# Kernel optimization log

Measured on AMD Instinct MI355X. Metric: run time of the kernel, lower is better.

Reference implementation:

```python
import jax, jax.numpy as jnp
import numpy as np

N_NODES = 100000
N_EDGES = 3200000
F_IN, H_ENC, H_GCN, H_Q, A_DIM = 128, 128, 128, 256, 10


def setup_inputs() -> dict:
    key = jax.random.key(0)
    ks = jax.random.split(key, 8)
    s = lambda d: 1.0 / np.sqrt(d)
    return {
        "x": jax.random.normal(ks[0], (N_NODES, F_IN), jnp.float32),
        "edge_index": jax.random.randint(ks[1], (2, N_EDGES), 0, N_NODES, jnp.int64),
        "W_enc": jax.random.normal(ks[2], (F_IN, H_ENC), jnp.float32) * s(F_IN),
        "b_enc": jnp.zeros((H_ENC,), jnp.float32),
        "W_gcn": jax.random.normal(ks[3], (H_ENC, H_GCN), jnp.float32) * s(H_ENC),
        "b_gcn": jnp.zeros((H_GCN,), jnp.float32),
        "W1": jax.random.normal(ks[4], (H_GCN, H_Q), jnp.float32) * s(H_GCN),
        "b1": jnp.zeros((H_Q,), jnp.float32),
        "W2": jax.random.normal(ks[5], (H_Q, A_DIM), jnp.float32) * s(H_Q),
        "b2": jnp.zeros((A_DIM,), jnp.float32),
    }


def gcn_conv(x, edge_index, W, b):
    # Standard GCNConv: D^{-1/2} (A + I) D^{-1/2} X W + b, symmetric norm with self-loops.
    n = x.shape[0]
    src, dst = edge_index[0], edge_index[1]
    xw = x @ W  # [N, H]
    deg = jnp.ones((n,), xw.dtype).at[dst].add(1.0)  # in-degree + self-loop
    dinv = jax.lax.rsqrt(deg)
    coef = dinv[src] * dinv[dst]  # [E]
    msg = xw[src] * coef[:, None]  # [E, H] gather-scale
    agg = jax.ops.segment_sum(msg, dst, num_segments=n)  # scatter-add
    agg = agg + xw * (dinv * dinv)[:, None]  # self-loop contribution
    return agg + b


def reference(x, edge_index, W_enc, b_enc, W_gcn, b_gcn, W1, b1, W2, b2):
    h = jax.nn.relu(x @ W_enc + b_enc)              # Encoder: Linear + ReLU
    h = jax.nn.relu(gcn_conv(h, edge_index, W_gcn, b_gcn))  # GCNConv + ReLU
    q = jax.nn.relu(h @ W1 + b1) @ W2 + b2          # Q_Net MLP
    return q
```

## Files before the change

### kernel.cpp

```cpp
#include <hip/hip_runtime.h>

#define N_NODES 100000
constexpr int F     = 128;
constexpr int NB    = (N_NODES + 63) / 64;
constexpr int BCAP  = 2560;
constexpr int LCAP  = 80;
constexpr int CHUNK = 8192;
constexpr int PADN  = N_NODES;

typedef __attribute__((ext_vector_type(8))) short short8;
typedef __attribute__((ext_vector_type(4))) float f32x4;
typedef __attribute__((ext_vector_type(4))) short short4v;
typedef __attribute__((ext_vector_type(4))) unsigned uint4v;

__device__ inline short f2bf(float v) {
    union { float f; unsigned u; } x; x.f = v;
    unsigned r = (x.u + 0x7fff + ((x.u >> 16) & 1)) >> 16;
    return (short)r;
}
__device__ inline float lo_bf(unsigned v) {
    union { unsigned u; float f; } x; x.u = v << 16; return x.f;
}
__device__ inline float hi_bf(unsigned v) {
    union { unsigned u; float f; } x; x.u = v & 0xffff0000u; return x.f;
}

__global__ __launch_bounds__(256) void prep_kernel(const float* __restrict__ W_enc,
                                                   const float* __restrict__ W_gcn,
                                                   const float* __restrict__ W1,
                                                   const float* __restrict__ W2,
                                                   short* __restrict__ Wte,
                                                   short* __restrict__ Wtg,
                                                   short* __restrict__ Wt1,
                                                   short* __restrict__ W2t,
                                                   int* __restrict__ bcr) {
    int idx = blockIdx.x * 256 + threadIdx.x;
    if (idx < 16384) { int h = idx >> 7, k = idx & 127; Wte[idx] = f2bf(W_enc[k * 128 + h]); return; }
    idx -= 16384;
    if (idx < 16384) { int h = idx >> 7, k = idx & 127; Wtg[idx] = f2bf(W_gcn[k * 128 + h]); return; }
    idx -= 16384;
    if (idx < 32768) { int h = idx >> 7, k = idx & 127; Wt1[idx] = f2bf(W1[k * 256 + h]); return; }
    idx -= 32768;
    if (idx < 4096)  { int n = idx >> 8, k = idx & 255; W2t[idx] = (n < 10) ? f2bf(W2[k * 10 + n]) : (short)0; return; }
    idx -= 4096;
    if (idx < NB) bcr[idx] = 0;
}

__global__ __launch_bounds__(512) void part_kernel(const int* __restrict__ src,
                                                   const int* __restrict__ dst,
                                                   int* __restrict__ bcur,
                                                   int* __restrict__ part, int E) {
    __shared__ int cnt[NB];
    __shared__ int base[NB];
    for (int b = threadIdx.x; b < NB; b += 512) cnt[b] = 0;
    __syncthreads();
    const int e0 = blockIdx.x * CHUNK;
    const int e1 = min(e0 + CHUNK, E);
#pragma unroll 4
    for (int e = e0 + threadIdx.x; e < e1; e += 512)
        atomicAdd(&cnt[dst[e] >> 6], 1);
    __syncthreads();
    for (int b = threadIdx.x; b < NB; b += 512) {
        int c = cnt[b];
        base[b] = c ? atomicAdd(&bcur[b], c) : 0;
        cnt[b] = 0;
    }
    __syncthreads();
#pragma unroll 4
    for (int e = e0 + threadIdx.x; e < e1; e += 512) {
        int d = dst[e];
        int b = d >> 6;
        int idx = base[b] + atomicAdd(&cnt[b], 1);
        if (idx < BCAP) part[b * BCAP + idx] = src[e] | ((d & 63) << 17);
    }
}

__global__ __launch_bounds__(256) void gemmA_kernel(const float* __restrict__ x,
                                                    const short* __restrict__ Wte,
                                                    const short* __restrict__ Wtg,
                                                    const float* __restrict__ b_enc,
                                                    const int* __restrict__ bcur,
                                                    const int* __restrict__ part,
                                                    short* __restrict__ xs) {
    __shared__ int deg_l[64];
    __shared__ short h_l[4][16][136];
    const int b = blockIdx.x;
    if (threadIdx.x < 64) deg_l[threadIdx.x] = 0;
    __syncthreads();
    const int cnt = min(bcur[b], BCAP);
    const int* p = part + (size_t)b * BCAP;
#pragma unroll 4
    for (int i = threadIdx.x; i < cnt; i += 256)
        atomicAdd(&deg_l[(p[i] >> 17) & 63], 1);

    const int wave = threadIdx.x >> 6;
    const int lane = threadIdx.x & 63;
    const int quad = lane >> 4;
    const int l16  = lane & 15;
    const int node0 = b * 64 + wave * 16;
    int nrow = node0 + l16;
    const bool valid = nrow < N_NODES;
    if (!valid) nrow = N_NODES - 1;

    f32x4 acc[8] = {};
#pragma unroll
    for (int kc = 0; kc < 4; ++kc) {
        const float* ap = x + (size_t)nrow * 128 + kc * 32 + quad * 8;
        float4 f0 = *reinterpret_cast<const float4*>(ap);
        float4 f1 = *reinterpret_cast<const float4*>(ap + 4);
        short8 xfrag;
        xfrag.s0 = f2bf(f0.x); xfrag.s1 = f2bf(f0.y); xfrag.s2 = f2bf(f0.z); xfrag.s3 = f2bf(f0.w);
        xfrag.s4 = f2bf(f1.x); xfrag.s5 = f2bf(f1.y); xfrag.s6 = f2bf(f1.z); xfrag.s7 = f2bf(f1.w);
#pragma unroll
        for (int t = 0; t < 8; ++t) {
            short8 wfrag = *reinterpret_cast<const short8*>(Wte + (size_t)(t * 16 + l16) * 128 + kc * 32 + quad * 8);
            acc[t] = __builtin_amdgcn_mfma_f32_16x16x32_bf16(wfrag, xfrag, acc[t], 0, 0, 0);
        }
    }
#pragma unroll
    for (int t = 0; t < 8; ++t) {
        short4v o;
#pragma unroll
        for (int r = 0; r < 4; ++r)
            ((short*)&o)[r] = f2bf(fmaxf(acc[t][r] + b_enc[t * 16 + quad * 4 + r], 0.f));
        *reinterpret_cast<short4v*>(&h_l[wave][l16][t * 16 + quad * 4]) = o;
    }
    __syncthreads();

    const float dvn = rsqrtf(1.f + (float)deg_l[wave * 16 + l16]);
    f32x4 acc2[8] = {};
#pragma unroll
    for (int kc = 0; kc < 4; ++kc) {
        short8 xfrag = *reinterpret_cast<const short8*>(&h_l[wave][l16][kc * 32 + quad * 8]);
#pragma unroll
        for (int t = 0; t < 8; ++t) {
            short8 wfrag = *reinterpret_cast<const short8*>(Wtg + (size_t)(t * 16 + l16) * 128 + kc * 32 + quad * 8);
            acc2[t] = __builtin_amdgcn_mfma_f32_16x16x32_bf16(wfrag, xfrag, acc2[t], 0, 0, 0);
        }
    }
    const int srow = node0 + l16;
#pragma unroll
    for (int t = 0; t < 8; ++t) {
        short4v o;
#pragma unroll
        for (int r = 0; r < 4; ++r)
            ((short*)&o)[r] = valid ? f2bf(acc2[t][r] * dvn) : (short)0;
        *reinterpret_cast<short4v*>(xs + (size_t)srow * 128 + t * 16 + quad * 4) = o;
    }
}

__global__ __launch_bounds__(512, 8) void agg_kernel(const short* __restrict__ xs,
                                                     const int* __restrict__ bcur,
                                                     const int* __restrict__ part,
                                                     const float* __restrict__ bg,
                                                     short* __restrict__ h2) {
    __shared__ int csr_l[64 * LCAP];
    __shared__ int cur[64];
    const int b = blockIdx.x;
    const int tid = threadIdx.x;
    if (tid < 64) cur[tid] = 0;
    __syncthreads();
    const int cnt = min(bcur[b], BCAP);
    const int* p = part + (size_t)b * BCAP;
#pragma unroll 4
    for (int i = tid; i < cnt; i += 512) {
        int v = p[i];
        int ld = (v >> 17) & 63;
        int pos = atomicAdd(&cur[ld], 1);
        if (pos < LCAP) csr_l[ld * LCAP + pos] = v & 0x1FFFF;
    }
    __syncthreads();
    if (tid < 64) {
        int d = min(cur[tid], LCAP);
        int dp = (d + 15) & ~15;
        for (int k = d; k < dp; ++k) csr_l[tid * LCAP + k] = PADN;
    }
    __syncthreads();

    const int wave = tid >> 6;
    const int lane = tid & 63;
    const int g    = lane >> 4;
    const int l16  = lane & 15;
    const uint4v* xs4 = reinterpret_cast<const uint4v*>(xs);
    const float4 bgA = reinterpret_cast<const float4*>(bg)[l16 * 2];
    const float4 bgB = reinterpret_cast<const float4*>(bg)[l16 * 2 + 1];

    for (int t = 0; t < 8; ++t) {
        const int ld = wave * 8 + t;
        const int node = b * 64 + ld;
        if (node >= N_NODES) break;

        const int dtrue = cur[ld];
        const int dpad = (min(dtrue, LCAP) + 15) & ~15;
        const float dv = rsqrtf(1.f + (float)dtrue);
        const int* cl = csr_l + ld * LCAP;

        float a0 = 0.f, a1 = 0.f, a2 = 0.f, a3 = 0.f, a4 = 0.f, a5 = 0.f, a6 = 0.f, a7 = 0.f;
        for (int j = 0; j < dpad; j += 16) {
            int s[4];
            uint4v v[4];
#pragma unroll
            for (int u = 0; u < 4; ++u) s[u] = cl[j + u * 4 + g];
#pragma unroll
            for (int u = 0; u < 4; ++u) v[u] = xs4[((size_t)s[u] << 4) + l16];
#pragma unroll
            for (int u = 0; u < 4; ++u) {
                a0 += lo_bf(v[u].x); a1 += hi_bf(v[u].x);
                a2 += lo_bf(v[u].y); a3 += hi_bf(v[u].y);
                a4 += lo_bf(v[u].z); a5 += hi_bf(v[u].z);
                a6 += lo_bf(v[u].w); a7 += hi_bf(v[u].w);
            }
        }
        a0 += __shfl_xor(a0, 16, 64); a0 += __shfl_xor(a0, 32, 64);
        a1 += __shfl_xor(a1, 16, 64); a1 += __shfl_xor(a1, 32, 64);
        a2 += __shfl_xor(a2, 16, 64); a2 += __shfl_xor(a2, 32, 64);
        a3 += __shfl_xor(a3, 16, 64); a3 += __shfl_xor(a3, 32, 64);
        a4 += __shfl_xor(a4, 16, 64); a4 += __shfl_xor(a4, 32, 64);
        a5 += __shfl_xor(a5, 16, 64); a5 += __shfl_xor(a5, 32, 64);
        a6 += __shfl_xor(a6, 16, 64); a6 += __shfl_xor(a6, 32, 64);
        a7 += __shfl_xor(a7, 16, 64); a7 += __shfl_xor(a7, 32, 64);
        if (g == 0) {
            uint4v vs = xs4[((size_t)node << 4) + l16];
            a0 += lo_bf(vs.x); a1 += hi_bf(vs.x);
            a2 += lo_bf(vs.y); a3 += hi_bf(vs.y);
            a4 += lo_bf(vs.z); a5 += hi_bf(vs.z);
            a6 += lo_bf(vs.w); a7 += hi_bf(vs.w);
            short8 o;
            o.s0 = f2bf(fmaxf(fmaf(a0, dv, bgA.x), 0.f));
            o.s1 = f2bf(fmaxf(fmaf(a1, dv, bgA.y), 0.f));
            o.s2 = f2bf(fmaxf(fmaf(a2, dv, bgA.z), 0.f));
            o.s3 = f2bf(fmaxf(fmaf(a3, dv, bgA.w), 0.f));
            o.s4 = f2bf(fmaxf(fmaf(a4, dv, bgB.x), 0.f));
            o.s5 = f2bf(fmaxf(fmaf(a5, dv, bgB.y), 0.f));
            o.s6 = f2bf(fmaxf(fmaf(a6, dv, bgB.z), 0.f));
            o.s7 = f2bf(fmaxf(fmaf(a7, dv, bgB.w), 0.f));
            *reinterpret_cast<short8*>(h2 + ((size_t)node << 7) + l16 * 8) = o;
        }
    }
}

__global__ __launch_bounds__(256) void gemmB_kernel(const short* __restrict__ h2,
                                                    const short* __restrict__ Wt1,
                                                    const short* __restrict__ W2t,
                                                    const float* __restrict__ b1,
                                                    const float* __restrict__ b2,
                                                    float* __restrict__ q) {
    __shared__ short hq_l[4][16][264];
    const int wave = threadIdx.x >> 6;
    const int lane = threadIdx.x & 63;
    const int quad = lane >> 4;
    const int l16  = lane & 15;
    const int node0 = blockIdx.x * 64 + wave * 16;
    int nrow = node0 + l16;
    if (nrow >= N_NODES) nrow = N_NODES - 1;

    f32x4 acc[16] = {};
#pragma unroll
    for (int kc = 0; kc < 4; ++kc) {
        short8 xfrag = *reinterpret_cast<const short8*>(h2 + (size_t)nrow * 128 + kc * 32 + quad * 8);
#pragma unroll
        for (int t = 0; t < 16; ++t) {
            short8 wfrag = *reinterpret_cast<const short8*>(Wt1 + (size_t)(t * 16 + l16) * 128 + kc * 32 + quad * 8);
            acc[t] = __builtin_amdgcn_mfma_f32_16x16x32_bf16(wfrag, xfrag, acc[t], 0, 0, 0);
        }
    }
#pragma unroll
    for (int t = 0; t < 16; ++t) {
        short4v o;
#pragma unroll
        for (int r = 0; r < 4; ++r)
            ((short*)&o)[r] = f2bf(fmaxf(acc[t][r] + b1[t * 16 + quad * 4 + r], 0.f));
        *reinterpret_cast<short4v*>(&hq_l[wave][l16][t * 16 + quad * 4]) = o;
    }

    f32x4 a2 = {};
#pragma unroll
    for (int kc = 0; kc < 8; ++kc) {
        short8 afrag = *reinterpret_cast<const short8*>(&hq_l[wave][l16][kc * 32 + quad * 8]);
        short8 bfrag = *reinterpret_cast<const short8*>(W2t + (size_t)l16 * 256 + kc * 32 + quad * 8);
        a2 = __builtin_amdgcn_mfma_f32_16x16x32_bf16(afrag, bfrag, a2, 0, 0, 0);
    }
    if (l16 < 10) {
        float bv = b2[l16];
#pragma unroll
        for (int r = 0; r < 4; ++r) {
            int nd = node0 + quad * 4 + r;
            if (nd < N_NODES) q[(size_t)nd * 10 + l16] = a2[r] + bv;
        }
    }
}

extern "C" void kernel_launch(void* const* d_in, const int* in_sizes, int n_in,
                              void* d_out, int out_size, void* d_ws, size_t ws_size,
                              hipStream_t stream) {
    const float* x     = (const float*)d_in[0];
    const int*   ei    = (const int*)d_in[1];
    const float* W_enc = (const float*)d_in[2];
    const float* b_enc = (const float*)d_in[3];
    const float* W_gcn = (const float*)d_in[4];
    const float* b_gcn = (const float*)d_in[5];
    const float* W1    = (const float*)d_in[6];
    const float* b1    = (const float*)d_in[7];
    const float* W2    = (const float*)d_in[8];
    const float* b2    = (const float*)d_in[9];
    float* q = (float*)d_out;

    const int E = in_sizes[1] / 2;
    const int* srcv = ei;
    const int* dstv = ei + E;

    char* ws = (char*)d_ws;
    const size_t XSB = (size_t)(NB * 64) * 128 * sizeof(short);
    short* xs  = (short*)(ws);
    short* h2  = (short*)(ws + XSB);
    int*   part= (int*)  (ws + 2 * XSB);
    char*  tail = ws + 2 * XSB + (size_t)NB * BCAP * sizeof(int);
    int*   bcr = (int*)(tail);
    short* Wte = (short*)(tail + 8192);
    short* Wtg = (short*)(tail + 8192 + 32768);
    short* Wt1 = (short*)(tail + 8192 + 65536);
    short* W2t = (short*)(tail + 8192 + 131072);

    prep_kernel<<<279, 256, 0, stream>>>(W_enc, W_gcn, W1, W2, Wte, Wtg, Wt1, W2t, bcr);
    part_kernel<<<(E + CHUNK - 1) / CHUNK, 512, 0, stream>>>(srcv, dstv, bcr, part, E);
    gemmA_kernel<<<NB, 256, 0, stream>>>(x, Wte, Wtg, b_enc, bcr, part, xs);
    agg_kernel<<<NB, 512, 0, stream>>>(xs, bcr, part, b_gcn, h2);
    gemmB_kernel<<<NB, 256, 0, stream>>>(h2, Wt1, W2t, b1, b2, q);
}
```

Baseline: 397.9 us.

## Cache edge data in registers during partition and double node rows in gemmB

The partition kernel now reads src/dst only once. It keeps the packed edge value and its local slot (bucket and position from the shared-memory atomic) in registers across the barrier. This removes the second global read pass and the second round of shared atomics, at the cost of 32 extra registers per thread. gemmB now processes 32 nodes per wave, so each W1 fragment load feeds two MFMAs, which halves weight-fragment traffic per node. In exchange it doubles accumulator register use and halves the number of blocks.

```diff
diff --git a/kernel.cpp b/kernel.cpp
--- a/kernel.cpp
+++ b/kernel.cpp
@@ -6,6 +6,7 @@
 constexpr int BCAP  = 2560;
 constexpr int LCAP  = 80;
 constexpr int CHUNK = 8192;
+constexpr int EPT   = CHUNK / 512;
 constexpr int PADN  = N_NODES;
 
 typedef __attribute__((ext_vector_type(8))) short short8;
@@ -46,32 +47,44 @@
     if (idx < NB) bcr[idx] = 0;
 }
 
-__global__ __launch_bounds__(512) void part_kernel(const int* __restrict__ src,
-                                                   const int* __restrict__ dst,
-                                                   int* __restrict__ bcur,
-                                                   int* __restrict__ part, int E) {
+__global__ __launch_bounds__(512, 4) void part_kernel(const int* __restrict__ src,
+                                                      const int* __restrict__ dst,
+                                                      int* __restrict__ bcur,
+                                                      int* __restrict__ part, int E) {
     __shared__ int cnt[NB];
     __shared__ int base[NB];
     for (int b = threadIdx.x; b < NB; b += 512) cnt[b] = 0;
     __syncthreads();
     const int e0 = blockIdx.x * CHUNK;
     const int e1 = min(e0 + CHUNK, E);
-#pragma unroll 4
-    for (int e = e0 + threadIdx.x; e < e1; e += 512)
-        atomicAdd(&cnt[dst[e] >> 6], 1);
+
+    int pk[EPT];
+    int meta[EPT];
+#pragma unroll
+    for (int i = 0; i < EPT; ++i) {
+        int e = e0 + i * 512 + (int)threadIdx.x;
+        meta[i] = -1;
+        if (e < e1) {
+            int d = dst[e];
+            int b = d >> 6;
+            pk[i] = src[e] | ((d & 63) << 17);
+            int pos = atomicAdd(&cnt[b], 1);
+            meta[i] = b | (pos << 11);
+        }
+    }
     __syncthreads();
     for (int b = threadIdx.x; b < NB; b += 512) {
         int c = cnt[b];
         base[b] = c ? atomicAdd(&bcur[b], c) : 0;
-        cnt[b] = 0;
-    }
-    __syncthreads();
-#pragma unroll 4
-    for (int e = e0 + threadIdx.x; e < e1; e += 512) {
-        int d = dst[e];
-        int b = d >> 6;
-        int idx = base[b] + atomicAdd(&cnt[b], 1);
-        if (idx < BCAP) part[b * BCAP + idx] = src[e] | ((d & 63) << 17);
+    }
+    __syncthreads();
+#pragma unroll
+    for (int i = 0; i < EPT; ++i) {
+        if (meta[i] >= 0) {
+            int b = meta[i] & 0x7FF;
+            int idx = base[b] + (meta[i] >> 11);
+            if (idx < BCAP) part[b * BCAP + idx] = pk[i];
+        }
     }
 }
 
@@ -250,42 +263,53 @@
     const int lane = threadIdx.x & 63;
     const int quad = lane >> 4;
     const int l16  = lane & 15;
-    const int node0 = blockIdx.x * 64 + wave * 16;
-    int nrow = node0 + l16;
-    if (nrow >= N_NODES) nrow = N_NODES - 1;
-
-    f32x4 acc[16] = {};
+    const int node0 = blockIdx.x * 128 + wave * 32;
+
+    int r0 = node0 + l16;
+    int r1 = node0 + 16 + l16;
+    if (r0 >= N_NODES) r0 = N_NODES - 1;
+    if (r1 >= N_NODES) r1 = N_NODES - 1;
+
+    f32x4 acc0[16] = {}, acc1[16] = {};
 #pragma unroll
     for (int kc = 0; kc < 4; ++kc) {
-        short8 xfrag = *reinterpret_cast<const short8*>(h2 + (size_t)nrow * 128 + kc * 32 + quad * 8);
+        short8 xf0 = *reinterpret_cast<const short8*>(h2 + (size_t)r0 * 128 + kc * 32 + quad * 8);
+        short8 xf1 = *reinterpret_cast<const short8*>(h2 + (size_t)r1 * 128 + kc * 32 + quad * 8);
 #pragma unroll
         for (int t = 0; t < 16; ++t) {
             short8 wfrag = *reinterpret_cast<const short8*>(Wt1 + (size_t)(t * 16 + l16) * 128 + kc * 32 + quad * 8);
-            acc[t] = __builtin_amdgcn_mfma_f32_16x16x32_bf16(wfrag, xfrag, acc[t], 0, 0, 0);
-        }
-    }
-#pragma unroll
-    for (int t = 0; t < 16; ++t) {
-        short4v o;
-#pragma unroll
-        for (int r = 0; r < 4; ++r)
-            ((short*)&o)[r] = f2bf(fmaxf(acc[t][r] + b1[t * 16 + quad * 4 + r], 0.f));
-        *reinterpret_cast<short4v*>(&hq_l[wave][l16][t * 16 + quad * 4]) = o;
-    }
-
-    f32x4 a2 = {};
-#pragma unroll
-    for (int kc = 0; kc < 8; ++kc) {
-        short8 afrag = *reinterpret_cast<const short8*>(&hq_l[wave][l16][kc * 32 + quad * 8]);
-        short8 bfrag = *reinterpret_cast<const short8*>(W2t + (size_t)l16 * 256 + kc * 32 + quad * 8);
-        a2 = __builtin_amdgcn_mfma_f32_16x16x32_bf16(afrag, bfrag, a2, 0, 0, 0);
-    }
-    if (l16 < 10) {
-        float bv = b2[l16];
-#pragma unroll
-        for (int r = 0; r < 4; ++r) {
-            int nd = node0 + quad * 4 + r;
-            if (nd < N_NODES) q[(size_t)nd * 10 + l16] = a2[r] + bv;
+            acc0[t] = __builtin_amdgcn_mfma_f32_16x16x32_bf16(wfrag, xf0, acc0[t], 0, 0, 0);
+            acc1[t] = __builtin_amdgcn_mfma_f32_16x16x32_bf16(wfrag, xf1, acc1[t], 0, 0, 0);
+        }
+    }
+
+#pragma unroll
+    for (int half = 0; half < 2; ++half) {
+        const f32x4* acc = half ? acc1 : acc0;
+        const int nb = node0 + half * 16;
+#pragma unroll
+        for (int t = 0; t < 16; ++t) {
+            short4v o;
+#pragma unroll
+            for (int r = 0; r < 4; ++r)
+                ((short*)&o)[r] = f2bf(fmaxf(acc[t][r] + b1[t * 16 + quad * 4 + r], 0.f));
+            *reinterpret_cast<short4v*>(&hq_l[wave][l16][t * 16 + quad * 4]) = o;
+        }
+
+        f32x4 a2 = {};
+#pragma unroll
+        for (int kc = 0; kc < 8; ++kc) {
+            short8 afrag = *reinterpret_cast<const short8*>(&hq_l[wave][l16][kc * 32 + quad * 8]);
+            short8 bfrag = *reinterpret_cast<const short8*>(W2t + (size_t)l16 * 256 + kc * 32 + quad * 8);
+            a2 = __builtin_amdgcn_mfma_f32_16x16x32_bf16(afrag, bfrag, a2, 0, 0, 0);
+        }
+        if (l16 < 10) {
+            float bv = b2[l16];
+#pragma unroll
+            for (int r = 0; r < 4; ++r) {
+                int nd = nb + quad * 4 + r;
+                if (nd < N_NODES) q[(size_t)nd * 10 + l16] = a2[r] + bv;
+            }
         }
     }
 }
@@ -325,5 +349,5 @@
     part_kernel<<<(E + CHUNK - 1) / CHUNK, 512, 0, stream>>>(srcv, dstv, bcr, part, E);
     gemmA_kernel<<<NB, 256, 0, stream>>>(x, Wte, Wtg, b_enc, bcr, part, xs);
     agg_kernel<<<NB, 512, 0, stream>>>(xs, bcr, part, b_gcn, h2);
-    gemmB_kernel<<<NB, 256, 0, stream>>>(h2, Wt1, W2t, b1, b2, q);
-}
+    gemmB_kernel<<<(N_NODES + 127) / 128, 256, 0, stream>>>(h2, Wt1, W2t, b1, b2, q);
+}
```

After: 388.0 us. -2.5%, faster.
